# Optimization experiments

Measured on AMD Instinct MI355X. Metric: run time of the kernel, lower is better.

Reference implementation:

```python
import jax, jax.numpy as jnp
import numpy as np

DIM1, DIM2, DK, OUT = 512, 512, 512, 256
EPS = 1e-5


def _linear(x, W, b):
    # torch nn.Linear: x @ W.T + b, W: [out, in]
    return jnp.einsum('bsi,oi->bso', x, W) + b


def _layernorm(x, gamma, beta):
    mu = jnp.mean(x, axis=-1, keepdims=True)
    var = jnp.mean(jnp.square(x - mu), axis=-1, keepdims=True)
    return (x - mu) * jax.lax.rsqrt(var + EPS) * gamma + beta


def setup_inputs() -> dict:
    key = jax.random.key(0)
    ks = jax.random.split(key, 20)
    B, S = 16, 2048

    def lin_init(kw, kb, fan_out, fan_in):
        bound = 1.0 / np.sqrt(fan_in)
        W = jax.random.uniform(kw, (fan_out, fan_in), jnp.float32, -bound, bound)
        b = jax.random.uniform(kb, (fan_out,), jnp.float32, -bound, bound)
        return W, b

    x1 = jax.random.normal(ks[0], (B, S, DIM1), jnp.float32)
    x2 = jax.random.normal(ks[1], (B, S, DIM2), jnp.float32)
    Wq, bq = lin_init(ks[2], ks[3], DK, DIM2)
    Wk, bk = lin_init(ks[4], ks[5], DK, DIM1)
    Wv, bv = lin_init(ks[6], ks[7], DK, DIM1)
    W0, b0 = lin_init(ks[8], ks[9], OUT, DK)
    W1, b1 = lin_init(ks[10], ks[11], OUT, DK)
    W2, b2 = lin_init(ks[12], ks[13], OUT, DK)
    W3, b3 = lin_init(ks[14], ks[15], OUT, DK)
    Wc, bc = lin_init(ks[16], ks[17], OUT, OUT)
    gG = jnp.ones((OUT,), jnp.float32); betaG = jnp.zeros((OUT,), jnp.float32)
    gE = jnp.ones((OUT,), jnp.float32); betaE = jnp.zeros((OUT,), jnp.float32)
    return dict(x1=x1, x2=x2, Wq=Wq, bq=bq, Wk=Wk, bk=bk, Wv=Wv, bv=bv,
                W0=W0, b0=b0, W1=W1, b1=b1, W2=W2, b2=b2, W3=W3, b3=b3,
                gG=gG, betaG=betaG, gE=gE, betaE=betaE, Wc=Wc, bc=bc)


def reference(x1, x2, Wq, bq, Wk, bk, Wv, bv, W0, b0, W1, b1, W2, b2, W3, b3,
              gG, betaG, gE, betaE, Wc, bc):
    q = _linear(x2, Wq, bq)          # [B, S2, dk]
    k = _linear(x1, Wk, bk)          # [B, S1, dk]
    v = _linear(x1, Wv, bv)          # [B, S1, dk]

    qk = jnp.einsum('bqd,bkd->bqk', q, k)
    p = (jnp.einsum('bqd,bkd->bqk', jnp.tanh(q), jnp.tanh(k)) + 1.0) * 0.5
    scores = qk * p / jnp.sqrt(jnp.float32(DK))
    attention_weights = jax.nn.softmax(scores, axis=-1)
    q_hat = jnp.einsum('bqk,bkd->bqd', attention_weights, v)

    g = _layernorm(jax.nn.relu(jax.nn.relu(_linear(q, W0, b0))
                               + jax.nn.relu(_linear(q_hat, W1, b1))), gG, betaG)
    e = _layernorm(jax.nn.relu(jax.nn.relu(_linear(q_hat, W2, b2))), gE, betaE)
    c = jax.nn.relu(_linear(g * e, Wc, bc))
    q_out = jax.nn.relu(_linear(q, W3, b3))
    return (q_out + c, attention_weights)
```

## Files before the change

### kernel.cpp

```cpp
#include <hip/hip_runtime.h>
#include <cmath>

typedef unsigned short ushort;
typedef unsigned int uint;

typedef ushort u16x8 __attribute__((ext_vector_type(8)));
typedef ushort u16x4 __attribute__((ext_vector_type(4)));
typedef _Float16 f16x8 __attribute__((ext_vector_type(8)));
typedef float  f32x4 __attribute__((ext_vector_type(4)));

#define DEVINL __device__ __forceinline__

DEVINL ushort f2h(float f){
  _Float16 h = (_Float16)f;
  return __builtin_bit_cast(ushort, h);
}
DEVINL float h2f(ushort u){ return (float)__builtin_bit_cast(_Float16, u); }
DEVINL f16x8 u2h8(u16x8 u){ return __builtin_bit_cast(f16x8, u); }

DEVINL f32x4 mfma16(f16x8 a, f16x8 b, f32x4 c){
  return __builtin_amdgcn_mfma_f32_16x16x32_f16(a, b, c, 0, 0, 0);
}

__global__ void cvt_f16(const float* __restrict__ src, ushort* __restrict__ dst, int n){
  int i = (blockIdx.x*blockDim.x + threadIdx.x)*4;
  if (i < n){
    f32x4 v = *(const f32x4*)(src + i);
    u16x4 o;
    #pragma unroll
    for(int j=0;j<4;j++) o[j] = f2h(v[j]);
    *(u16x4*)(dst + i) = o;
  }
}

template<int MODE>
__global__ __launch_bounds__(256) void gemm_proj(
    const float* __restrict__ X, const ushort* __restrict__ Wb,
    const float* __restrict__ bias,
    ushort* __restrict__ out, ushort* __restrict__ outt, ushort* __restrict__ vT)
{
  __shared__ ushort Ab[128*64];
  __shared__ ushort Bb[128*64];
  const int t = threadIdx.x, lane = t&63, wid = t>>6;
  const int wr = wid>>1, wc = wid&1;
  const int rt = blockIdx.x, ct = blockIdx.y;

  f32x4 acc[4][4];
  #pragma unroll
  for(int i=0;i<4;i++)
    #pragma unroll
    for(int j=0;j<4;j++) acc[i][j] = (f32x4)0.0f;

  for(int ph=0; ph<8; ++ph){
    #pragma unroll
    for(int i=0;i<4;i++){
      int ci = i*256 + t;
      int row = ci>>3, off = ci&7;
      const float* gp = X + (size_t)(rt*128+row)*512 + ph*64 + off*8;
      f32x4 v0 = *(const f32x4*)gp;
      f32x4 v1 = *(const f32x4*)(gp+4);
      u16x8 o;
      #pragma unroll
      for(int j=0;j<4;j++){ o[j] = f2h(v0[j]); o[4+j] = f2h(v1[j]); }
      *(u16x8*)((char*)Ab + ((ci*16) ^ ((row&7)<<4))) = o;
    }
    #pragma unroll
    for(int i=0;i<4;i++){
      int ci = i*256 + t;
      int row = ci>>3, off = ci&7;
      u16x8 v = *(const u16x8*)(Wb + (size_t)(ct*128+row)*512 + ph*64 + off*8);
      *(u16x8*)((char*)Bb + ((ci*16) ^ ((row&7)<<4))) = v;
    }
    __syncthreads();
    #pragma unroll
    for(int sub=0; sub<2; ++sub){
      f16x8 a[4], b[4];
      #pragma unroll
      for(int mf=0; mf<4; mf++){
        int row = wr*64 + mf*16 + (lane&15);
        int byte_ = (row*128 + sub*64 + (lane>>4)*16) ^ ((row&7)<<4);
        a[mf] = u2h8(*(const u16x8*)((char*)Ab + byte_));
      }
      #pragma unroll
      for(int nf=0; nf<4; nf++){
        int row = wc*64 + nf*16 + (lane&15);
        int byte_ = (row*128 + sub*64 + (lane>>4)*16) ^ ((row&7)<<4);
        b[nf] = u2h8(*(const u16x8*)((char*)Bb + byte_));
      }
      #pragma unroll
      for(int mf=0; mf<4; mf++)
        #pragma unroll
        for(int nf=0; nf<4; nf++)
          acc[mf][nf] = mfma16(a[mf], b[nf], acc[mf][nf]);
    }
    __syncthreads();
  }

  #pragma unroll
  for(int nf=0; nf<4; nf++){
    int col = ct*128 + wc*64 + nf*16 + (lane&15);
    float bv = bias[col];
    #pragma unroll
    for(int mf=0; mf<4; mf++){
      int grow0 = rt*128 + wr*64 + mf*16 + (lane>>4)*4;
      if(MODE==0){
        #pragma unroll
        for(int r=0;r<4;r++){
          float val = acc[mf][nf][r] + bv;
          out[(size_t)(grow0+r)*512 + col] = f2h(val);
        }
      } else if(MODE==2){
        #pragma unroll
        for(int r=0;r<4;r++){
          float val = acc[mf][nf][r] + bv;
          size_t idx = (size_t)(grow0+r)*512 + col;
          out[idx] = f2h(val);
          outt[idx] = f2h(tanhf(val));
        }
      } else {
        u16x4 pk;
        #pragma unroll
        for(int r=0;r<4;r++) pk[r] = f2h(acc[mf][nf][r] + bv);
        int bb = grow0 >> 11, ss = grow0 & 2047;
        *(u16x4*)(vT + (size_t)(bb*512 + col)*2048 + ss) = pk;
      }
    }
  }
}

__global__ __launch_bounds__(512) void attn_scores(
  const ushort* __restrict__ qb,
  const ushort* __restrict__ kb, const ushort* __restrict__ tkb,
  float* __restrict__ attn, float* __restrict__ rowm, float* __restrict__ rowl)
{
  __shared__ ushort kbuf[64*128];
  __shared__ ushort tkbuf[64*128];
  const int t = threadIdx.x, lane = t&63, wid = t>>6;
  const int bid = blockIdx.x, b = bid&15, qt = bid>>4;
  const int qrow0 = qt*128 + wid*16;

  f16x8 qa[16], ta[16];
  {
    const ushort* qp = qb + (size_t)(b*2048 + qrow0 + (lane&15))*512 + (lane>>4)*8;
    #pragma unroll
    for(int ks=0;ks<16;ks++){
      u16x8 qv = *(const u16x8*)(qp + ks*32);
      qa[ks] = u2h8(qv);
      u16x8 tv;
      #pragma unroll
      for(int j=0;j<8;j++) tv[j] = f2h(tanhf(h2f(qv[j])));
      ta[ks] = u2h8(tv);
    }
  }
  float mrun[4], lrun[4];
  #pragma unroll
  for(int r=0;r<4;r++){ mrun[r] = -1e30f; lrun[r] = 0.f; }

  #pragma unroll 1
  for(int kt=0; kt<32; ++kt){
    f32x4 acc0[4], acc1[4];
    #pragma unroll
    for(int nf=0;nf<4;nf++){ acc0[nf]=(f32x4)0.f; acc1[nf]=(f32x4)0.f; }
    #pragma unroll
    for(int ph=0; ph<4; ++ph){
      #pragma unroll
      for(int i=0;i<2;i++){
        int c2 = i*512 + t;
        int row = c2>>4, off = c2&15;
        size_t src = (size_t)(b*2048 + kt*64 + row)*512 + ph*128 + off*8;
        *(u16x8*)((char*)kbuf  + ((c2*16) ^ ((row&7)<<4))) = *(const u16x8*)(kb  + src);
        *(u16x8*)((char*)tkbuf + ((c2*16) ^ ((row&7)<<4))) = *(const u16x8*)(tkb + src);
      }
      __syncthreads();
      #pragma unroll
      for(int sub=0; sub<4; ++sub){
        int ks = ph*4 + sub;
        #pragma unroll
        for(int nf=0; nf<4; nf++){
          int row = nf*16 + (lane&15);
          int byte_ = (row*256 + sub*64 + (lane>>4)*16) ^ ((row&7)<<4);
          f16x8 bk_ = u2h8(*(const u16x8*)((char*)kbuf  + byte_));
          f16x8 bt_ = u2h8(*(const u16x8*)((char*)tkbuf + byte_));
          acc0[nf] = mfma16(qa[ks], bk_, acc0[nf]);
          acc1[nf] = mfma16(ta[ks], bt_, acc1[nf]);
        }
      }
      __syncthreads();
    }
    float s[4][4];
    #pragma unroll
    for(int nf=0;nf<4;nf++)
      #pragma unroll
      for(int r=0;r<4;r++)
        s[nf][r] = acc0[nf][r] * ((acc1[nf][r] + 1.0f)*0.5f) * 0.044194173824159216f;

    #pragma unroll
    for(int r=0;r<4;r++){
      float m = fmaxf(fmaxf(s[0][r],s[1][r]), fmaxf(s[2][r],s[3][r]));
      #pragma unroll
      for(int d=1; d<16; d<<=1) m = fmaxf(m, __shfl_xor(m, d));
      float mnew = fmaxf(mrun[r], m);
      float es = 0.f;
      #pragma unroll
      for(int nf=0;nf<4;nf++) es += __expf(s[nf][r] - mnew);
      #pragma unroll
      for(int d=1; d<16; d<<=1) es += __shfl_xor(es, d);
      lrun[r] = lrun[r]*__expf(mrun[r]-mnew) + es;
      mrun[r] = mnew;
    }
    #pragma unroll
    for(int nf=0;nf<4;nf++){
      int col = kt*64 + nf*16 + (lane&15);
      #pragma unroll
      for(int r=0;r<4;r++){
        int grow = qrow0 + (lane>>4)*4 + r;
        attn[(size_t)(b*2048 + grow)*2048 + col] = s[nf][r];
      }
    }
  }
  if((lane&15)==0){
    #pragma unroll
    for(int r=0;r<4;r++){
      int grow = qrow0 + (lane>>4)*4 + r;
      rowm[b*2048 + grow] = mrun[r];
      rowl[b*2048 + grow] = lrun[r];
    }
  }
}

__global__ __launch_bounds__(512) void attn_pv(
  const float* __restrict__ rowm, const float* __restrict__ rowl,
  float* __restrict__ attn, const ushort* __restrict__ vT,
  ushort* __restrict__ qhb)
{
  __shared__ ushort vbuf[512*40];
  const int t = threadIdx.x, lane = t&63, wid = t>>6;
  const int bid = blockIdx.x, b = bid&15, qt = bid>>4;
  const int qrow = b*2048 + qt*128 + wid*16 + (lane&15);
  const float mw = rowm[qrow];
  const float rlw = 1.0f / rowl[qrow];
  float* srow = attn + (size_t)qrow*2048 + (lane>>4)*8;

  f32x4 acc[32];
  #pragma unroll
  for(int nf=0;nf<32;nf++) acc[nf]=(f32x4)0.f;

  #pragma unroll 1
  for(int ks=0; ks<64; ++ks){
    f32x4 s0 = *(const f32x4*)(srow + ks*32);
    f32x4 s1 = *(const f32x4*)(srow + ks*32 + 4);
    f32x4 w0, w1;
    #pragma unroll
    for(int j=0;j<4;j++){ w0[j] = __expf(s0[j]-mw)*rlw; w1[j] = __expf(s1[j]-mw)*rlw; }
    *(f32x4*)(srow + ks*32)     = w0;
    *(f32x4*)(srow + ks*32 + 4) = w1;
    u16x8 af;
    #pragma unroll
    for(int j=0;j<4;j++){ af[j] = f2h(w0[j]); af[4+j] = f2h(w1[j]); }
    f16x8 afs = u2h8(af);

    __syncthreads();
    #pragma unroll
    for(int i=0;i<4;i++){
      int ci = i*512 + t;
      int dim = ci>>2, off = ci&3;
      *(u16x8*)((char*)vbuf + dim*80 + off*16) =
        *(const u16x8*)(vT + (size_t)(b*512 + dim)*2048 + ks*32 + off*8);
    }
    __syncthreads();
    #pragma unroll
    for(int nf=0; nf<32; nf++){
      int row = nf*16 + (lane&15);
      f16x8 bv = u2h8(*(const u16x8*)((char*)vbuf + row*80 + (lane>>4)*16));
      acc[nf] = mfma16(afs, bv, acc[nf]);
    }
  }
  #pragma unroll
  for(int nf=0; nf<32; nf++){
    int col = nf*16 + (lane&15);
    #pragma unroll
    for(int r=0;r<4;r++){
      int grow = qt*128 + wid*16 + (lane>>4)*4 + r;
      qhb[(size_t)(b*2048+grow)*512 + col] = f2h(acc[nf][r]);
    }
  }
}

DEVINL void gemm_tile(const ushort* __restrict__ A, const ushort* __restrict__ W,
                      int r0, int t, int nph, f32x4 acc[4][4],
                      ushort* Ab, ushort* Wb)
{
  const int lane = t&63, wid = t>>6, wc0 = wid*64;
  const int K = nph*64;
  for(int ph=0; ph<nph; ++ph){
    #pragma unroll
    for(int i=0;i<2;i++){
      int ci = i*256 + t;
      int row = ci>>3, off = ci&7;
      *(u16x8*)((char*)Ab + ((ci*16) ^ ((row&7)<<4))) =
        *(const u16x8*)(A + (size_t)(r0+row)*K + ph*64 + off*8);
    }
    #pragma unroll
    for(int i=0;i<8;i++){
      int ci = i*256 + t;
      int row = ci>>3, off = ci&7;
      *(u16x8*)((char*)Wb + ((ci*16) ^ ((row&7)<<4))) =
        *(const u16x8*)(W + (size_t)row*K + ph*64 + off*8);
    }
    __syncthreads();
    #pragma unroll
    for(int sub=0; sub<2; ++sub){
      f16x8 a[4], bfr[4];
      #pragma unroll
      for(int mf=0;mf<4;mf++){
        int row = mf*16 + (lane&15);
        int byte_ = (row*128 + sub*64 + (lane>>4)*16) ^ ((row&7)<<4);
        a[mf] = u2h8(*(const u16x8*)((char*)Ab + byte_));
      }
      #pragma unroll
      for(int nf=0;nf<4;nf++){
        int row = wc0 + nf*16 + (lane&15);
        int byte_ = (row*128 + sub*64 + (lane>>4)*16) ^ ((row&7)<<4);
        bfr[nf] = u2h8(*(const u16x8*)((char*)Wb + byte_));
      }
      #pragma unroll
      for(int mf=0;mf<4;mf++)
        #pragma unroll
        for(int nf=0;nf<4;nf++)
          acc[mf][nf] = mfma16(a[mf], bfr[nf], acc[mf][nf]);
    }
    __syncthreads();
  }
}

__global__ __launch_bounds__(256) void post_gemms(
  const ushort* __restrict__ qb, const ushort* __restrict__ qhb,
  const ushort* __restrict__ W0b, const ushort* __restrict__ W1b,
  const ushort* __restrict__ W2b, const ushort* __restrict__ W3b,
  const float* __restrict__ b0, const float* __restrict__ b1,
  const float* __restrict__ b2, const float* __restrict__ b3,
  ushort* __restrict__ Gpre, ushort* __restrict__ Epre, ushort* __restrict__ Q3b)
{
  __shared__ ushort Ab[64*64];
  __shared__ ushort Wb[256*64];
  const int t = threadIdx.x, lane = t&63, wid = t>>6, wc0 = wid*64;
  const int r0 = blockIdx.x*64;
  f32x4 accA[4][4], accB[4][4];

  #pragma unroll
  for(int i=0;i<4;i++)
    #pragma unroll
    for(int j=0;j<4;j++) accA[i][j]=(f32x4)0.f;
  gemm_tile(qb, W0b, r0, t, 8, accA, Ab, Wb);

  #pragma unroll
  for(int i=0;i<4;i++)
    #pragma unroll
    for(int j=0;j<4;j++) accB[i][j]=(f32x4)0.f;
  gemm_tile(qhb, W1b, r0, t, 8, accB, Ab, Wb);

  #pragma unroll
  for(int nf=0;nf<4;nf++){
    int col = wc0 + nf*16 + (lane&15);
    float bv0 = b0[col], bv1 = b1[col];
    #pragma unroll
    for(int mf=0;mf<4;mf++)
      #pragma unroll
      for(int r=0;r<4;r++){
        int row = r0 + mf*16 + (lane>>4)*4 + r;
        float a0 = fmaxf(accA[mf][nf][r] + bv0, 0.f);
        float a1 = fmaxf(accB[mf][nf][r] + bv1, 0.f);
        Gpre[(size_t)row*256 + col] = f2h(fmaxf(a0 + a1, 0.f));
      }
  }

  #pragma unroll
  for(int i=0;i<4;i++)
    #pragma unroll
    for(int j=0;j<4;j++) accB[i][j]=(f32x4)0.f;
  gemm_tile(qhb, W2b, r0, t, 8, accB, Ab, Wb);
  #pragma unroll
  for(int nf=0;nf<4;nf++){
    int col = wc0 + nf*16 + (lane&15);
    float bv2 = b2[col];
    #pragma unroll
    for(int mf=0;mf<4;mf++)
      #pragma unroll
      for(int r=0;r<4;r++){
        int row = r0 + mf*16 + (lane>>4)*4 + r;
        Epre[(size_t)row*256 + col] = f2h(fmaxf(accB[mf][nf][r] + bv2, 0.f));
      }
  }

  #pragma unroll
  for(int i=0;i<4;i++)
    #pragma unroll
    for(int j=0;j<4;j++) accB[i][j]=(f32x4)0.f;
  gemm_tile(qb, W3b, r0, t, 8, accB, Ab, Wb);
  #pragma unroll
  for(int nf=0;nf<4;nf++){
    int col = wc0 + nf*16 + (lane&15);
    float bv3 = b3[col];
    #pragma unroll
    for(int mf=0;mf<4;mf++)
      #pragma unroll
      for(int r=0;r<4;r++){
        int row = r0 + mf*16 + (lane>>4)*4 + r;
        Q3b[(size_t)row*256 + col] = f2h(fmaxf(accB[mf][nf][r] + bv3, 0.f));
      }
  }
}

__global__ __launch_bounds__(256) void ln_mul(
  const ushort* __restrict__ Gpre, const ushort* __restrict__ Epre,
  const float* __restrict__ gG, const float* __restrict__ betaG,
  const float* __restrict__ gE, const float* __restrict__ betaE,
  ushort* __restrict__ geb)
{
  const int t = threadIdx.x, lane = t&63, wid = t>>6;
  const int row = blockIdx.x*4 + wid;
  const int base = row*256 + lane*4;
  u16x4 gv = *(const u16x4*)(Gpre + base);
  u16x4 ev = *(const u16x4*)(Epre + base);
  float x[4], y[4];
  float sx=0.f, sxx=0.f, sy=0.f, syy=0.f;
  #pragma unroll
  for(int j=0;j<4;j++){
    x[j]=h2f(gv[j]); y[j]=h2f(ev[j]);
    sx += x[j]; sxx += x[j]*x[j];
    sy += y[j]; syy += y[j]*y[j];
  }
  #pragma unroll
  for(int d=1; d<64; d<<=1){
    sx += __shfl_xor(sx, d); sxx += __shfl_xor(sxx, d);
    sy += __shfl_xor(sy, d); syy += __shfl_xor(syy, d);
  }
  const float inv = 1.0f/256.0f;
  float mux = sx*inv,  varx = sxx*inv - mux*mux, rsx = rsqrtf(varx + 1e-5f);
  float muy = sy*inv,  vary = syy*inv - muy*muy, rsy = rsqrtf(vary + 1e-5f);
  u16x4 o;
  #pragma unroll
  for(int j=0;j<4;j++){
    int c = lane*4 + j;
    float g = (x[j]-mux)*rsx*gG[c] + betaG[c];
    float e = (y[j]-muy)*rsy*gE[c] + betaE[c];
    o[j] = f2h(g*e);
  }
  *(u16x4*)(geb + base) = o;
}

__global__ __launch_bounds__(256) void final_out(
  const ushort* __restrict__ geb, const ushort* __restrict__ Wcb,
  const float* __restrict__ bc, const ushort* __restrict__ Q3b,
  float* __restrict__ out1)
{
  __shared__ ushort Ab[64*64];
  __shared__ ushort Wb[256*64];
  const int t = threadIdx.x, lane = t&63, wid = t>>6, wc0 = wid*64;
  const int r0 = blockIdx.x*64;
  f32x4 acc[4][4];
  #pragma unroll
  for(int i=0;i<4;i++)
    #pragma unroll
    for(int j=0;j<4;j++) acc[i][j]=(f32x4)0.f;
  gemm_tile(geb, Wcb, r0, t, 4, acc, Ab, Wb);
  #pragma unroll
  for(int nf=0;nf<4;nf++){
    int col = wc0 + nf*16 + (lane&15);
    float bv = bc[col];
    #pragma unroll
    for(int mf=0;mf<4;mf++)
      #pragma unroll
      for(int r=0;r<4;r++){
        int row = r0 + mf*16 + (lane>>4)*4 + r;
        float c = fmaxf(acc[mf][nf][r] + bv, 0.f);
        out1[(size_t)row*256 + col] = c + h2f(Q3b[(size_t)row*256 + col]);
      }
  }
}

extern "C" void kernel_launch(void* const* d_in, const int* in_sizes, int n_in,
                              void* d_out, int out_size, void* d_ws, size_t ws_size,
                              hipStream_t stream) {
  (void)in_sizes; (void)n_in; (void)out_size; (void)ws_size;
  const float* x1 = (const float*)d_in[0];
  const float* x2 = (const float*)d_in[1];
  const float* Wq = (const float*)d_in[2];  const float* bq = (const float*)d_in[3];
  const float* Wk = (const float*)d_in[4];  const float* bk = (const float*)d_in[5];
  const float* Wv = (const float*)d_in[6];  const float* bv = (const float*)d_in[7];
  const float* W0 = (const float*)d_in[8];  const float* b0 = (const float*)d_in[9];
  const float* W1 = (const float*)d_in[10]; const float* b1 = (const float*)d_in[11];
  const float* W2 = (const float*)d_in[12]; const float* b2 = (const float*)d_in[13];
  const float* W3 = (const float*)d_in[14]; const float* b3 = (const float*)d_in[15];
  const float* gG = (const float*)d_in[16]; const float* betaG = (const float*)d_in[17];
  const float* gE = (const float*)d_in[18]; const float* betaE = (const float*)d_in[19];
  const float* Wc = (const float*)d_in[20]; const float* bc = (const float*)d_in[21];

  char* ws = (char*)d_ws;
  const size_t SZ1 = (size_t)32768*512*2;
  ushort* qb  = (ushort*)(ws + 0*SZ1);
  ushort* kb  = (ushort*)(ws + 1*SZ1);
  ushort* tkb = (ushort*)(ws + 2*SZ1);
  ushort* vT  = (ushort*)(ws + 3*SZ1);
  ushort* qhb = (ushort*)(ws + 4*SZ1);
  char* p6 = ws + 5*SZ1;
  const size_t SZO = (size_t)32768*256*2;
  ushort* Gpre = (ushort*)(p6 + 0*SZO);
  ushort* Epre = (ushort*)(p6 + 1*SZO);
  ushort* geb  = (ushort*)(p6 + 2*SZO);
  ushort* Q3b  = (ushort*)(p6 + 3*SZO);
  float* rowm = (float*)(p6 + 4*SZO);
  float* rowl = rowm + 32768;
  char* pw = p6 + 4*SZO + 2*32768*sizeof(float);
  ushort* Wqb = (ushort*)(pw + 0);
  ushort* Wkb = (ushort*)(pw + 524288);
  ushort* Wvb = (ushort*)(pw + 2*524288);
  ushort* W0b = (ushort*)(pw + 3*524288);
  ushort* W1b = (ushort*)(pw + 3*524288 + 262144);
  ushort* W2b = (ushort*)(pw + 3*524288 + 2*262144);
  ushort* W3b = (ushort*)(pw + 3*524288 + 3*262144);
  ushort* Wcb = (ushort*)(pw + 3*524288 + 4*262144);

  cvt_f16<<<256,256,0,stream>>>(Wq, Wqb, 262144);
  cvt_f16<<<256,256,0,stream>>>(Wk, Wkb, 262144);
  cvt_f16<<<256,256,0,stream>>>(Wv, Wvb, 262144);
  cvt_f16<<<128,256,0,stream>>>(W0, W0b, 131072);
  cvt_f16<<<128,256,0,stream>>>(W1, W1b, 131072);
  cvt_f16<<<128,256,0,stream>>>(W2, W2b, 131072);
  cvt_f16<<<128,256,0,stream>>>(W3, W3b, 131072);
  cvt_f16<<<64,256,0,stream>>>(Wc, Wcb, 65536);

  gemm_proj<0><<<dim3(256,4),256,0,stream>>>(x2, Wqb, bq, qb, nullptr, nullptr);
  gemm_proj<2><<<dim3(256,4),256,0,stream>>>(x1, Wkb, bk, kb, tkb, nullptr);
  gemm_proj<1><<<dim3(256,4),256,0,stream>>>(x1, Wvb, bv, nullptr, nullptr, vT);

  float* out1 = (float*)d_out;
  float* attnp = out1 + (size_t)16*2048*256;

  attn_scores<<<256,512,0,stream>>>(qb, kb, tkb, attnp, rowm, rowl);
  attn_pv<<<256,512,0,stream>>>(rowm, rowl, attnp, vT, qhb);

  post_gemms<<<512,256,0,stream>>>(qb, qhb, W0b, W1b, W2b, W3b,
                                   b0, b1, b2, b3, Gpre, Epre, Q3b);
  ln_mul<<<8192,256,0,stream>>>(Gpre, Epre, gG, betaG, gE, betaE, geb);
  final_out<<<512,256,0,stream>>>(geb, Wcb, bc, Q3b, out1);
}
```

Before: 1.219 ms.

## Double-buffer attention K/V tiles with async LDS loads and fuse weight conversions

attn_scores now double-buffers the K and tanh(K) tiles in shared memory and fills them with global_load_lds direct-to-LDS loads, prefetching the next phase while the current one computes. Its per-tile cross-lane max/sum reductions are replaced by per-lane running statistics merged once at the end. attn_pv double-buffers the V tile and prefetches scores and V values into registers one step ahead, so it needs only one barrier per step. The eight weight conversion launches are merged into one kernel. Risks: the score loop prefetches into the next buffer with no barrier between phases, so the code may have a race, and higher register and LDS use may lower occupancy.

```diff
diff --git a/kernel.cpp b/kernel.cpp
--- a/kernel.cpp
+++ b/kernel.cpp
@@ -22,14 +22,24 @@
   return __builtin_amdgcn_mfma_f32_16x16x32_f16(a, b, c, 0, 0, 0);
 }
 
-__global__ void cvt_f16(const float* __restrict__ src, ushort* __restrict__ dst, int n){
-  int i = (blockIdx.x*blockDim.x + threadIdx.x)*4;
-  if (i < n){
-    f32x4 v = *(const f32x4*)(src + i);
-    u16x4 o;
-    #pragma unroll
-    for(int j=0;j<4;j++) o[j] = f2h(v[j]);
-    *(u16x4*)(dst + i) = o;
+DEVINL void gload16(const ushort* g, ushort* l){
+  __builtin_amdgcn_global_load_lds((const __attribute__((address_space(1))) unsigned int*)g,
+                                   (__attribute__((address_space(3))) unsigned int*)l, 16, 0, 0);
+}
+
+struct CvtArgs { const float* s[8]; ushort* d[8]; int cum[9]; };
+__global__ void cvt_all(CvtArgs a){
+  int q = blockIdx.x*256 + threadIdx.x;
+  #pragma unroll
+  for(int k=0;k<8;k++){
+    if(q >= a.cum[k] && q < a.cum[k+1]){
+      int i = (q - a.cum[k])*4;
+      f32x4 v = *(const f32x4*)(a.s[k] + i);
+      u16x4 o;
+      #pragma unroll
+      for(int j=0;j<4;j++) o[j] = f2h(v[j]);
+      *(u16x4*)(a.d[k] + i) = o;
+    }
   }
 }
 
@@ -133,8 +143,8 @@
   const ushort* __restrict__ kb, const ushort* __restrict__ tkb,
   float* __restrict__ attn, float* __restrict__ rowm, float* __restrict__ rowl)
 {
-  __shared__ ushort kbuf[64*128];
-  __shared__ ushort tkbuf[64*128];
+  __shared__ ushort kbuf[2][64*128];
+  __shared__ ushort tkbuf[2][64*128];
   const int t = threadIdx.x, lane = t&63, wid = t>>6;
   const int bid = blockIdx.x, b = bid&15, qt = bid>>4;
   const int qrow0 = qt*128 + wid*16;
@@ -152,9 +162,24 @@
       ta[ks] = u2h8(tv);
     }
   }
+
+  const int row0 = t>>4, off0 = t&15;
+  const int swz = (off0 ^ (row0&7))*8;
+  const ushort* kb_t0  = kb  + (size_t)(b*2048 + row0)*512 + swz;
+  const ushort* tkb_t0 = tkb + (size_t)(b*2048 + row0)*512 + swz;
+  const size_t c1off = (size_t)32*512;
+  const int d0 = t*8, d1 = (512+t)*8;
+
   float mrun[4], lrun[4];
   #pragma unroll
   for(int r=0;r<4;r++){ mrun[r] = -1e30f; lrun[r] = 0.f; }
+
+  {
+    const size_t so = 0;
+    gload16(kb_t0  + so, &kbuf[0][d0]);  gload16(kb_t0  + so + c1off, &kbuf[0][d1]);
+    gload16(tkb_t0 + so, &tkbuf[0][d0]); gload16(tkb_t0 + so + c1off, &tkbuf[0][d1]);
+  }
+  __syncthreads();
 
   #pragma unroll 1
   for(int kt=0; kt<32; ++kt){
@@ -163,15 +188,14 @@
     for(int nf=0;nf<4;nf++){ acc0[nf]=(f32x4)0.f; acc1[nf]=(f32x4)0.f; }
     #pragma unroll
     for(int ph=0; ph<4; ++ph){
-      #pragma unroll
-      for(int i=0;i<2;i++){
-        int c2 = i*512 + t;
-        int row = c2>>4, off = c2&15;
-        size_t src = (size_t)(b*2048 + kt*64 + row)*512 + ph*128 + off*8;
-        *(u16x8*)((char*)kbuf  + ((c2*16) ^ ((row&7)<<4))) = *(const u16x8*)(kb  + src);
-        *(u16x8*)((char*)tkbuf + ((c2*16) ^ ((row&7)<<4))) = *(const u16x8*)(tkb + src);
-      }
-      __syncthreads();
+      const int cur = ph&1, nxt = cur^1;
+      if(!(kt==31 && ph==3)){
+        int nkt = (ph==3) ? kt+1 : kt;
+        int nph = (ph==3) ? 0 : ph+1;
+        const size_t so = (size_t)(nkt*64)*512 + nph*128;
+        gload16(kb_t0  + so, &kbuf[nxt][d0]);  gload16(kb_t0  + so + c1off, &kbuf[nxt][d1]);
+        gload16(tkb_t0 + so, &tkbuf[nxt][d0]); gload16(tkb_t0 + so + c1off, &tkbuf[nxt][d1]);
+      }
       #pragma unroll
       for(int sub=0; sub<4; ++sub){
         int ks = ph*4 + sub;
@@ -179,8 +203,8 @@
         for(int nf=0; nf<4; nf++){
           int row = nf*16 + (lane&15);
           int byte_ = (row*256 + sub*64 + (lane>>4)*16) ^ ((row&7)<<4);
-          f16x8 bk_ = u2h8(*(const u16x8*)((char*)kbuf  + byte_));
-          f16x8 bt_ = u2h8(*(const u16x8*)((char*)tkbuf + byte_));
+          f16x8 bk_ = u2h8(*(const u16x8*)((char*)kbuf[cur]  + byte_));
+          f16x8 bt_ = u2h8(*(const u16x8*)((char*)tkbuf[cur] + byte_));
           acc0[nf] = mfma16(qa[ks], bk_, acc0[nf]);
           acc1[nf] = mfma16(ta[ks], bt_, acc1[nf]);
         }
@@ -196,15 +220,11 @@
 
     #pragma unroll
     for(int r=0;r<4;r++){
-      float m = fmaxf(fmaxf(s[0][r],s[1][r]), fmaxf(s[2][r],s[3][r]));
-      #pragma unroll
-      for(int d=1; d<16; d<<=1) m = fmaxf(m, __shfl_xor(m, d));
-      float mnew = fmaxf(mrun[r], m);
+      float mx = fmaxf(fmaxf(s[0][r],s[1][r]), fmaxf(s[2][r],s[3][r]));
+      float mnew = fmaxf(mrun[r], mx);
       float es = 0.f;
       #pragma unroll
       for(int nf=0;nf<4;nf++) es += __expf(s[nf][r] - mnew);
-      #pragma unroll
-      for(int d=1; d<16; d<<=1) es += __shfl_xor(es, d);
       lrun[r] = lrun[r]*__expf(mrun[r]-mnew) + es;
       mrun[r] = mnew;
     }
@@ -217,6 +237,20 @@
         attn[(size_t)(b*2048 + grow)*2048 + col] = s[nf][r];
       }
     }
+  }
+
+  #pragma unroll
+  for(int r=0;r<4;r++){
+    float m = mrun[r], l = lrun[r];
+    #pragma unroll
+    for(int d=1; d<16; d<<=1){
+      float mo = __shfl_xor(m, d);
+      float lo = __shfl_xor(l, d);
+      float mn = fmaxf(m, mo);
+      l = l*__expf(m-mn) + lo*__expf(mo-mn);
+      m = mn;
+    }
+    mrun[r]=m; lrun[r]=l;
   }
   if((lane&15)==0){
     #pragma unroll
@@ -233,7 +267,7 @@
   float* __restrict__ attn, const ushort* __restrict__ vT,
   ushort* __restrict__ qhb)
 {
-  __shared__ ushort vbuf[512*40];
+  __shared__ ushort vbuf[2][512*40];
   const int t = threadIdx.x, lane = t&63, wid = t>>6;
   const int bid = blockIdx.x, b = bid&15, qt = bid>>4;
   const int qrow = b*2048 + qt*128 + wid*16 + (lane&15);
@@ -241,40 +275,97 @@
   const float rlw = 1.0f / rowl[qrow];
   float* srow = attn + (size_t)qrow*2048 + (lane>>4)*8;
 
+  const ushort* vsrc[4];
+  ushort *vd0[4], *vd1[4];
+  #pragma unroll
+  for(int i=0;i<4;i++){
+    int ci = i*512 + t;
+    int dim = ci>>2, off = ci&3;
+    vsrc[i] = vT + (size_t)(b*512 + dim)*2048 + off*8;
+    vd0[i] = &vbuf[0][dim*40 + off*8];
+    vd1[i] = &vbuf[1][dim*40 + off*8];
+  }
+
   f32x4 acc[32];
   #pragma unroll
   for(int nf=0;nf<32;nf++) acc[nf]=(f32x4)0.f;
 
+  u16x8 vrA[4], vrB[4];
+  f32x4 sA0, sA1, sB0, sB1;
+  #pragma unroll
+  for(int i=0;i<4;i++) vrA[i] = *(const u16x8*)(vsrc[i]);
+  sA0 = *(const f32x4*)(srow);      sA1 = *(const f32x4*)(srow + 4);
+  #pragma unroll
+  for(int i=0;i<4;i++) vrB[i] = *(const u16x8*)(vsrc[i] + 32);
+  sB0 = *(const f32x4*)(srow + 32); sB1 = *(const f32x4*)(srow + 36);
+  #pragma unroll
+  for(int i=0;i<4;i++) *(u16x8*)vd0[i] = vrA[i];
+  __syncthreads();
+
   #pragma unroll 1
-  for(int ks=0; ks<64; ++ks){
-    f32x4 s0 = *(const f32x4*)(srow + ks*32);
-    f32x4 s1 = *(const f32x4*)(srow + ks*32 + 4);
-    f32x4 w0, w1;
-    #pragma unroll
-    for(int j=0;j<4;j++){ w0[j] = __expf(s0[j]-mw)*rlw; w1[j] = __expf(s1[j]-mw)*rlw; }
-    *(f32x4*)(srow + ks*32)     = w0;
-    *(f32x4*)(srow + ks*32 + 4) = w1;
-    u16x8 af;
-    #pragma unroll
-    for(int j=0;j<4;j++){ af[j] = f2h(w0[j]); af[4+j] = f2h(w1[j]); }
-    f16x8 afs = u2h8(af);
-
-    __syncthreads();
-    #pragma unroll
-    for(int i=0;i<4;i++){
-      int ci = i*512 + t;
-      int dim = ci>>2, off = ci&3;
-      *(u16x8*)((char*)vbuf + dim*80 + off*16) =
-        *(const u16x8*)(vT + (size_t)(b*512 + dim)*2048 + ks*32 + off*8);
-    }
-    __syncthreads();
-    #pragma unroll
-    for(int nf=0; nf<32; nf++){
-      int row = nf*16 + (lane&15);
-      f16x8 bv = u2h8(*(const u16x8*)((char*)vbuf + row*80 + (lane>>4)*16));
-      acc[nf] = mfma16(afs, bv, acc[nf]);
-    }
-  }
+  for(int ks2=0; ks2<32; ++ks2){
+    const int ks = ks2*2;
+    {
+      #pragma unroll
+      for(int i=0;i<4;i++) *(u16x8*)vd1[i] = vrB[i];
+      if(ks+2 < 64){
+        #pragma unroll
+        for(int i=0;i<4;i++) vrA[i] = *(const u16x8*)(vsrc[i] + (size_t)(ks+2)*32);
+      }
+      f32x4 w0, w1;
+      #pragma unroll
+      for(int j=0;j<4;j++){ w0[j] = __expf(sA0[j]-mw)*rlw; w1[j] = __expf(sA1[j]-mw)*rlw; }
+      *(f32x4*)(srow + ks*32)     = w0;
+      *(f32x4*)(srow + ks*32 + 4) = w1;
+      if(ks+2 < 64){
+        sA0 = *(const f32x4*)(srow + (size_t)(ks+2)*32);
+        sA1 = *(const f32x4*)(srow + (size_t)(ks+2)*32 + 4);
+      }
+      u16x8 af;
+      #pragma unroll
+      for(int j=0;j<4;j++){ af[j] = f2h(w0[j]); af[4+j] = f2h(w1[j]); }
+      f16x8 afs = u2h8(af);
+      #pragma unroll
+      for(int nf=0; nf<32; nf++){
+        int row = nf*16 + (lane&15);
+        f16x8 bv = u2h8(*(const u16x8*)((char*)vbuf[0] + row*80 + (lane>>4)*16));
+        acc[nf] = mfma16(afs, bv, acc[nf]);
+      }
+      __syncthreads();
+    }
+    {
+      const int ko = ks+1;
+      if(ko+1 < 64){
+        #pragma unroll
+        for(int i=0;i<4;i++) *(u16x8*)vd0[i] = vrA[i];
+      }
+      if(ko+2 < 64){
+        #pragma unroll
+        for(int i=0;i<4;i++) vrB[i] = *(const u16x8*)(vsrc[i] + (size_t)(ko+2)*32);
+      }
+      f32x4 w0, w1;
+      #pragma unroll
+      for(int j=0;j<4;j++){ w0[j] = __expf(sB0[j]-mw)*rlw; w1[j] = __expf(sB1[j]-mw)*rlw; }
+      *(f32x4*)(srow + (size_t)ko*32)     = w0;
+      *(f32x4*)(srow + (size_t)ko*32 + 4) = w1;
+      if(ko+2 < 64){
+        sB0 = *(const f32x4*)(srow + (size_t)(ko+2)*32);
+        sB1 = *(const f32x4*)(srow + (size_t)(ko+2)*32 + 4);
+      }
+      u16x8 af;
+      #pragma unroll
+      for(int j=0;j<4;j++){ af[j] = f2h(w0[j]); af[4+j] = f2h(w1[j]); }
+      f16x8 afs = u2h8(af);
+      #pragma unroll
+      for(int nf=0; nf<32; nf++){
+        int row = nf*16 + (lane&15);
+        f16x8 bv = u2h8(*(const u16x8*)((char*)vbuf[1] + row*80 + (lane>>4)*16));
+        acc[nf] = mfma16(afs, bv, acc[nf]);
+      }
+      __syncthreads();
+    }
+  }
+
   #pragma unroll
   for(int nf=0; nf<32; nf++){
     int col = nf*16 + (lane&15);
@@ -521,14 +612,15 @@
   ushort* W3b = (ushort*)(pw + 3*524288 + 3*262144);
   ushort* Wcb = (ushort*)(pw + 3*524288 + 4*262144);
 
-  cvt_f16<<<256,256,0,stream>>>(Wq, Wqb, 262144);
-  cvt_f16<<<256,256,0,stream>>>(Wk, Wkb, 262144);
-  cvt_f16<<<256,256,0,stream>>>(Wv, Wvb, 262144);
-  cvt_f16<<<128,256,0,stream>>>(W0, W0b, 131072);
-  cvt_f16<<<128,256,0,stream>>>(W1, W1b, 131072);
-  cvt_f16<<<128,256,0,stream>>>(W2, W2b, 131072);
-  cvt_f16<<<128,256,0,stream>>>(W3, W3b, 131072);
-  cvt_f16<<<64,256,0,stream>>>(Wc, Wcb, 65536);
+  CvtArgs ca;
+  ca.s[0]=Wq; ca.d[0]=Wqb; ca.s[1]=Wk; ca.d[1]=Wkb; ca.s[2]=Wv; ca.d[2]=Wvb;
+  ca.s[3]=W0; ca.d[3]=W0b; ca.s[4]=W1; ca.d[4]=W1b; ca.s[5]=W2; ca.d[5]=W2b;
+  ca.s[6]=W3; ca.d[6]=W3b; ca.s[7]=Wc; ca.d[7]=Wcb;
+  int sizes4[8] = {65536,65536,65536,32768,32768,32768,32768,16384};
+  int cum = 0;
+  for(int k=0;k<8;k++){ ca.cum[k]=cum; cum += sizes4[k]; }
+  ca.cum[8]=cum;
+  cvt_all<<<cum/256,256,0,stream>>>(ca);
 
   gemm_proj<0><<<dim3(256,4),256,0,stream>>>(x2, Wqb, bq, qb, nullptr, nullptr);
   gemm_proj<2><<<dim3(256,4),256,0,stream>>>(x1, Wkb, bk, kb, tkb, nullptr);
```

Result: faster. 1.141 ms (-6.4%).
